# Kernel tuning notes

Measured on AMD Instinct MI355X. Metric: run time of the kernel, lower is better.

## Reference

```python
import jax, jax.numpy as jnp
import numpy as np

N_ATOMS = 200_000
N_EDGES = 6_400_000
N_IMAGES = 128


def setup_inputs() -> dict:
    key = jax.random.key(0)
    k1, k2, k3, k4, k5 = jax.random.split(key, 5)
    edge_diff = jax.random.normal(k1, (N_EDGES, 3), dtype=jnp.float32)
    dE_ddiff = jax.random.normal(k2, (N_EDGES, 3), dtype=jnp.float32)
    # cells: perturbed identity cells so volumes are well-conditioned
    cell = jnp.eye(3, dtype=jnp.float32) * 10.0 + 0.1 * jax.random.normal(
        k3, (N_IMAGES, 3, 3), dtype=jnp.float32)
    edge_idx = jax.random.randint(k4, (N_EDGES, 2), 0, N_ATOMS, dtype=jnp.int64)
    image_idx = jnp.sort(jax.random.randint(k5, (N_ATOMS,), 0, N_IMAGES, dtype=jnp.int64))
    return {"edge_diff": edge_diff, "dE_ddiff": dE_ddiff, "cell": cell,
            "edge_idx": edge_idx, "image_idx": image_idx}


def reference(edge_diff, dE_ddiff, cell, edge_idx, image_idx):
    idx_i = edge_idx[:, 0]
    idx_j = edge_idx[:, 1]
    # forces: scatter-add +dE to i atoms and -dE to j atoms
    i_forces = jax.ops.segment_sum(dE_ddiff, idx_i, num_segments=N_ATOMS)
    j_forces = jax.ops.segment_sum(-dE_ddiff, idx_j, num_segments=N_ATOMS)
    forces = i_forces + j_forces  # [N_ATOMS, 3]
    # per-edge virial outer product, scattered to atoms then to images
    edge_virial = edge_diff[:, :, None] * dE_ddiff[:, None, :]  # [E,3,3]
    atomic_virial = jax.ops.segment_sum(edge_virial, idx_i, num_segments=N_ATOMS)
    virial = jax.ops.segment_sum(atomic_virial, image_idx, num_segments=N_IMAGES)  # [B,3,3]
    # cell volumes: a . (b x c)
    volumes = jnp.sum(cell[:, 0] * jnp.cross(cell[:, 1], cell[:, 2]), axis=-1)  # [B]
    stress = -virial / volumes[:, None, None]
    return forces, virial, stress
```

## Files before the change

### kernel.cpp

```cpp
#include <hip/hip_runtime.h>
#include <hip/hip_fp16.h>


typedef unsigned int uint;
typedef unsigned short ushort;

#define SLICES  256
#define BASHIFT 8
#define NBCAP   1024
#define NVMAX   1152

__device__ __forceinline__ uint2 pack_entry(float dx, float dy, float dz, uint local) {
    const __half2 hxy = __floats2half2_rn(dx, dy);
    const ushort  hz  = __half_as_ushort(__float2half_rn(dz));
    uint2 r;
    r.x = *(const uint*)&hxy;
    r.y = (uint)hz | (local << 16);
    return r;
}

__global__ __launch_bounds__(1024) void k_count(
    const int2* __restrict__ edge_idx, uint* __restrict__ counts,
    int n_edges, int es, int nb)
{
    __shared__ uint hist[NBCAP];
    for (int t = threadIdx.x; t < nb; t += blockDim.x) hist[t] = 0;
    __syncthreads();
    const int s  = blockIdx.x;
    const int e0 = s * es;
    const int e1 = min(n_edges, e0 + es);
    for (int e = e0 + threadIdx.x; e < e1; e += blockDim.x) {
        const int2 ij = edge_idx[e];
        atomicAdd(&hist[((uint)ij.x) >> BASHIFT], 1u);
        atomicAdd(&hist[((uint)ij.y) >> BASHIFT], 1u);
    }
    __syncthreads();
    for (int b = threadIdx.x; b < nb; b += blockDim.x)
        counts[(size_t)b * SLICES + s] = hist[b];
}

__global__ __launch_bounds__(SLICES) void k_rowsum(
    const uint* __restrict__ counts, uint* __restrict__ rowsum)
{
    __shared__ uint red[SLICES];
    const int b = blockIdx.x;
    red[threadIdx.x] = counts[(size_t)b * SLICES + threadIdx.x];
    __syncthreads();
    for (int off = SLICES / 2; off > 0; off >>= 1) {
        if (threadIdx.x < off) red[threadIdx.x] += red[threadIdx.x + off];
        __syncthreads();
    }
    if (threadIdx.x == 0) rowsum[b] = red[0];
}

__global__ __launch_bounds__(1024) void k_scan_rows(
    const uint* __restrict__ rowsum, uint* __restrict__ rowoff, int nb)
{
    __shared__ uint psum[1024];
    const int t = threadIdx.x;
    psum[t] = (t < nb) ? rowsum[t] : 0u;
    __syncthreads();
    for (int off = 1; off < 1024; off <<= 1) {
        uint v = (t >= off) ? psum[t - off] : 0u;
        __syncthreads();
        psum[t] += v;
        __syncthreads();
    }
    if (t < nb) rowoff[t] = (t == 0) ? 0u : psum[t - 1];
}

__global__ __launch_bounds__(SLICES) void k_rowscan(
    uint* __restrict__ counts, const uint* __restrict__ rowoff)
{
    __shared__ uint psum[SLICES];
    const int b = blockIdx.x;
    const int t = threadIdx.x;
    const uint c = counts[(size_t)b * SLICES + t];
    psum[t] = c;
    __syncthreads();
    for (int off = 1; off < SLICES; off <<= 1) {
        uint v = (t >= off) ? psum[t - off] : 0u;
        __syncthreads();
        psum[t] += v;
        __syncthreads();
    }
    counts[(size_t)b * SLICES + t] = rowoff[b] + psum[t] - c;
}

__global__ __launch_bounds__(1024) void k_scatter(
    const float* __restrict__ edge_diff, const float* __restrict__ dE_ddiff,
    const int2* __restrict__ edge_idx, const int* __restrict__ image_idx,
    const uint* __restrict__ offsets, uint2* __restrict__ entries,
    float* __restrict__ virial , int n_edges, int es, int nb, int nv)
{
    __shared__ uint  cur[NBCAP];
    __shared__ float lv[NVMAX];
    const int s = blockIdx.x;
    for (int t = threadIdx.x; t < nb; t += blockDim.x)
        cur[t] = offsets[(size_t)t * SLICES + s];
    for (int t = threadIdx.x; t < nv; t += blockDim.x) lv[t] = 0.f;
    __syncthreads();

    const int e0 = s * es;
    const int e1 = min(n_edges, e0 + es);
    for (int e = e0 + threadIdx.x; e < e1; e += blockDim.x) {
        const int2 ij = edge_idx[e];
        const float dx = dE_ddiff[3*e + 0];
        const float dy = dE_ddiff[3*e + 1];
        const float dz = dE_ddiff[3*e + 2];

        const uint ai = (uint)ij.x, aj = (uint)ij.y;
        const uint pi = atomicAdd(&cur[ai >> BASHIFT], 1u);
        entries[pi] = pack_entry(dx, dy, dz, ai & ((1u << BASHIFT) - 1u));
        const uint pj = atomicAdd(&cur[aj >> BASHIFT], 1u);
        entries[pj] = pack_entry(-dx, -dy, -dz, aj & ((1u << BASHIFT) - 1u));

        const float ex = edge_diff[3*e + 0];
        const float ey = edge_diff[3*e + 1];
        const float ez = edge_diff[3*e + 2];
        float* v = &lv[image_idx[ai] * 9];
        atomicAdd(&v[0], ex*dx); atomicAdd(&v[1], ex*dy); atomicAdd(&v[2], ex*dz);
        atomicAdd(&v[3], ey*dx); atomicAdd(&v[4], ey*dy); atomicAdd(&v[5], ey*dz);
        atomicAdd(&v[6], ez*dx); atomicAdd(&v[7], ez*dy); atomicAdd(&v[8], ez*dz);
    }
    __syncthreads();
    for (int t = threadIdx.x; t < nv; t += blockDim.x) {
        const float val = lv[t];
        if (val != 0.f) unsafeAtomicAdd(&virial[t], val);
    }
}

__global__ __launch_bounds__(256) void k_gather(
    const uint2* __restrict__ entries, const uint* __restrict__ offsets,
    float* __restrict__ forces, int n_atoms, int nb, uint total)
{
    __shared__ float tile[3 << BASHIFT];
    const int q = blockIdx.x;
    for (int t = threadIdx.x; t < (3 << BASHIFT); t += blockDim.x) tile[t] = 0.f;
    __syncthreads();

    const uint beg = offsets[(size_t)q * SLICES];
    const uint end = (q + 1 < nb) ? offsets[(size_t)(q + 1) * SLICES] : total;
    for (uint k = beg + threadIdx.x; k < end; k += blockDim.x) {
        const uint2 ent = entries[k];
        const float2 xy = __half22float2(*(const __half2*)&ent.x);
        const float  z  = __half2float(__ushort_as_half((ushort)(ent.y & 0xffffu)));
        const uint local = ent.y >> 16;
        atomicAdd(&tile[local*3 + 0], xy.x);
        atomicAdd(&tile[local*3 + 1], xy.y);
        atomicAdd(&tile[local*3 + 2], z);
    }
    __syncthreads();

    const int base = q << BASHIFT;
    const int lim3 = min(n_atoms - base, 1 << BASHIFT) * 3;
    for (int t = threadIdx.x; t < lim3; t += blockDim.x)
        forces[(size_t)base * 3 + t] = tile[t];
}

__global__ void k_stress(const float* __restrict__ cell,
                         const float* __restrict__ virial,
                         float* __restrict__ stress, int n_images)
{
    const int t = blockIdx.x * blockDim.x + threadIdx.x;
    if (t >= n_images * 9) return;
    const float* c = &cell[(t / 9) * 9];
    const float crx = c[4]*c[8] - c[5]*c[7];
    const float cry = c[5]*c[6] - c[3]*c[8];
    const float crz = c[3]*c[7] - c[4]*c[6];
    const float vol = c[0]*crx + c[1]*cry + c[2]*crz;
    stress[t] = virial[t] * (-1.0f / vol);
}

__global__ __launch_bounds__(256) void edge_kernel_fb(
    const float* __restrict__ edge_diff, const float* __restrict__ dE_ddiff,
    const int2* __restrict__ edge_idx, const int* __restrict__ image_idx,
    float* __restrict__ forces, float* __restrict__ virial,
    int n_edges, int n_images)
{
    extern __shared__ float lds_v[];
    const int nv = n_images * 9;
    for (int t = threadIdx.x; t < nv; t += blockDim.x) lds_v[t] = 0.f;
    __syncthreads();
    const int stride = gridDim.x * blockDim.x;
    for (int e = blockIdx.x * blockDim.x + threadIdx.x; e < n_edges; e += stride) {
        const int2 ij = edge_idx[e];
        const int i = ij.x, j = ij.y;
        const float dx = dE_ddiff[3*e+0], dy = dE_ddiff[3*e+1], dz = dE_ddiff[3*e+2];
        unsafeAtomicAdd(&forces[3*i+0],  dx);
        unsafeAtomicAdd(&forces[3*i+1],  dy);
        unsafeAtomicAdd(&forces[3*i+2],  dz);
        unsafeAtomicAdd(&forces[3*j+0], -dx);
        unsafeAtomicAdd(&forces[3*j+1], -dy);
        unsafeAtomicAdd(&forces[3*j+2], -dz);
        const float ex = edge_diff[3*e+0], ey = edge_diff[3*e+1], ez = edge_diff[3*e+2];
        float* v = &lds_v[image_idx[i] * 9];
        atomicAdd(&v[0], ex*dx); atomicAdd(&v[1], ex*dy); atomicAdd(&v[2], ex*dz);
        atomicAdd(&v[3], ey*dx); atomicAdd(&v[4], ey*dy); atomicAdd(&v[5], ey*dz);
        atomicAdd(&v[6], ez*dx); atomicAdd(&v[7], ez*dy); atomicAdd(&v[8], ez*dz);
    }
    __syncthreads();
    for (int t = threadIdx.x; t < nv; t += blockDim.x) {
        const float val = lds_v[t];
        if (val != 0.f) unsafeAtomicAdd(&virial[t], val);
    }
}

extern "C" void kernel_launch(void* const* d_in, const int* in_sizes, int n_in,
                              void* d_out, int out_size, void* d_ws, size_t ws_size,
                              hipStream_t stream)
{
    const float* edge_diff = (const float*)d_in[0];
    const float* dE_ddiff  = (const float*)d_in[1];
    const float* cell      = (const float*)d_in[2];
    const int2*  edge_idx  = (const int2*)d_in[3];
    const int*   image_idx = (const int*)d_in[4];

    const int n_edges  = in_sizes[0] / 3;
    const int n_images = in_sizes[2] / 9;
    const int n_atoms  = in_sizes[4];
    const int nv       = n_images * 9;

    float* out    = (float*)d_out;
    float* forces = out;
    float* virial = out + (size_t)n_atoms * 3;
    float* stress = virial + nv;

    const int nb = (n_atoms + (1 << BASHIFT) - 1) >> BASHIFT;
    const int es = (n_edges + SLICES - 1) / SLICES;
    const uint total = (uint)(2 * (size_t)n_edges);

    const size_t entries_bytes = (size_t)total * sizeof(uint2);
    const size_t counts_bytes  = (size_t)nb * SLICES * sizeof(uint);
    const size_t aux_bytes     = 2 * (size_t)NBCAP * sizeof(uint);
    const size_t need = entries_bytes + counts_bytes + aux_bytes;

    if (ws_size >= need && nb <= NBCAP && nv <= NVMAX) {
        uint2* entries = (uint2*)d_ws;
        uint*  offsets = (uint*)((char*)d_ws + entries_bytes);
        uint*  rowsum  = offsets + (size_t)nb * SLICES;
        uint*  rowoff  = rowsum + NBCAP;

        hipMemsetAsync(virial, 0, nv * sizeof(float), stream);

        k_count<<<SLICES, 1024, 0, stream>>>(edge_idx, offsets, n_edges, es, nb);
        k_rowsum<<<nb, SLICES, 0, stream>>>(offsets, rowsum);
        k_scan_rows<<<1, 1024, 0, stream>>>(rowsum, rowoff, nb);
        k_rowscan<<<nb, SLICES, 0, stream>>>(offsets, rowoff);
        k_scatter<<<SLICES, 1024, 0, stream>>>(edge_diff, dE_ddiff, edge_idx, image_idx,
                                               offsets, entries, virial, n_edges, es, nb, nv);
        k_gather<<<nb, 256, 0, stream>>>(entries, offsets, forces, n_atoms, nb, total);
        k_stress<<<(nv + 255) / 256, 256, 0, stream>>>(cell, virial, stress, n_images);
    } else {
        hipMemsetAsync(out, 0, ((size_t)n_atoms * 3 + nv) * sizeof(float), stream);
        edge_kernel_fb<<<2048, 256, nv * sizeof(float), stream>>>(
            edge_diff, dE_ddiff, edge_idx, image_idx, forces, virial, n_edges, n_images);
        k_stress<<<(nv + 255) / 256, 256, 0, stream>>>(cell, virial, stress, n_images);
    }
}
```

Baseline: 731.8 us.

## Stage scatter entries in shared memory by bucket before global writes; per-wave gather tiles

The scatter kernel now processes edges in chunks of 4096. It counts entries per bucket in shared memory, prefix-sums the counts, and sorts the packed entries locally so the global writes to each bucket come out contiguous instead of random. The aim is fewer scattered global stores, paid for with more shared memory, a 1024-step scan and extra barriers per chunk. The gather kernel also gives each wave its own shared accumulation tile, summed at the end, to reduce LDS atomic contention.

```diff
diff --git a/kernel.cpp b/kernel.cpp
--- a/kernel.cpp
+++ b/kernel.cpp
@@ -9,6 +9,8 @@
 #define BASHIFT 8
 #define NBCAP   1024
 #define NVMAX   1152
+#define CHUNK_E 4096
+#define CHUNK_ENT (2*CHUNK_E)
 
 __device__ __forceinline__ uint2 pack_entry(float dx, float dy, float dz, uint local) {
     const __half2 hxy = __floats2half2_rn(dx, dy);
@@ -93,38 +95,94 @@
     const uint* __restrict__ offsets, uint2* __restrict__ entries,
     float* __restrict__ virial , int n_edges, int es, int nb, int nv)
 {
-    __shared__ uint  cur[NBCAP];
+    __shared__ uint2 s_ent[CHUNK_ENT];
+    __shared__ uint  s_dst[CHUNK_ENT];
+    __shared__ uint  cnt[NBCAP];
+    __shared__ uint  base[NBCAP];
+    __shared__ uint  tmp[1024];
+    __shared__ uint  gcur[NBCAP];
     __shared__ float lv[NVMAX];
-    const int s = blockIdx.x;
-    for (int t = threadIdx.x; t < nb; t += blockDim.x)
-        cur[t] = offsets[(size_t)t * SLICES + s];
-    for (int t = threadIdx.x; t < nv; t += blockDim.x) lv[t] = 0.f;
+
+    const int s   = blockIdx.x;
+    const int tid = threadIdx.x;
+
+    for (int t = tid; t < nb; t += 1024) gcur[t] = offsets[(size_t)t * SLICES + s];
+    for (int t = tid; t < nv; t += 1024) lv[t] = 0.f;
     __syncthreads();
 
     const int e0 = s * es;
     const int e1 = min(n_edges, e0 + es);
-    for (int e = e0 + threadIdx.x; e < e1; e += blockDim.x) {
-        const int2 ij = edge_idx[e];
-        const float dx = dE_ddiff[3*e + 0];
-        const float dy = dE_ddiff[3*e + 1];
-        const float dz = dE_ddiff[3*e + 2];
-
-        const uint ai = (uint)ij.x, aj = (uint)ij.y;
-        const uint pi = atomicAdd(&cur[ai >> BASHIFT], 1u);
-        entries[pi] = pack_entry(dx, dy, dz, ai & ((1u << BASHIFT) - 1u));
-        const uint pj = atomicAdd(&cur[aj >> BASHIFT], 1u);
-        entries[pj] = pack_entry(-dx, -dy, -dz, aj & ((1u << BASHIFT) - 1u));
-
-        const float ex = edge_diff[3*e + 0];
-        const float ey = edge_diff[3*e + 1];
-        const float ez = edge_diff[3*e + 2];
-        float* v = &lv[image_idx[ai] * 9];
-        atomicAdd(&v[0], ex*dx); atomicAdd(&v[1], ex*dy); atomicAdd(&v[2], ex*dz);
-        atomicAdd(&v[3], ey*dx); atomicAdd(&v[4], ey*dy); atomicAdd(&v[5], ey*dz);
-        atomicAdd(&v[6], ez*dx); atomicAdd(&v[7], ez*dy); atomicAdd(&v[8], ez*dz);
-    }
-    __syncthreads();
-    for (int t = threadIdx.x; t < nv; t += blockDim.x) {
+
+    for (int clo = e0; clo < e1; clo += CHUNK_E) {
+        const int chi  = min(e1, clo + CHUNK_E);
+        const int nent = 2 * (chi - clo);
+
+        cnt[tid] = 0;
+        __syncthreads();
+
+        uint2 ent_i[4], ent_j[4];
+        uint  bi[4], bj[4], ri[4], rj[4];
+        #pragma unroll
+        for (int k = 0; k < 4; ++k) {
+            const int e = clo + (k << 10) + tid;
+            bi[k] = 0xffffffffu;
+            if (e < chi) {
+                const int2 ij = edge_idx[e];
+                const float dx = dE_ddiff[3*e + 0];
+                const float dy = dE_ddiff[3*e + 1];
+                const float dz = dE_ddiff[3*e + 2];
+                const uint ai = (uint)ij.x, aj = (uint)ij.y;
+                bi[k] = ai >> BASHIFT;
+                bj[k] = aj >> BASHIFT;
+                ent_i[k] = pack_entry( dx,  dy,  dz, ai & ((1u << BASHIFT) - 1u));
+                ent_j[k] = pack_entry(-dx, -dy, -dz, aj & ((1u << BASHIFT) - 1u));
+                ri[k] = atomicAdd(&cnt[bi[k]], 1u);
+                rj[k] = atomicAdd(&cnt[bj[k]], 1u);
+
+                const float ex = edge_diff[3*e + 0];
+                const float ey = edge_diff[3*e + 1];
+                const float ez = edge_diff[3*e + 2];
+                float* v = &lv[image_idx[ai] * 9];
+                atomicAdd(&v[0], ex*dx); atomicAdd(&v[1], ex*dy); atomicAdd(&v[2], ex*dz);
+                atomicAdd(&v[3], ey*dx); atomicAdd(&v[4], ey*dy); atomicAdd(&v[5], ey*dz);
+                atomicAdd(&v[6], ez*dx); atomicAdd(&v[7], ez*dy); atomicAdd(&v[8], ez*dz);
+            }
+        }
+        __syncthreads();
+
+        const uint c0 = cnt[tid];
+        tmp[tid] = c0;
+        __syncthreads();
+        for (int off = 1; off < 1024; off <<= 1) {
+            const uint v = (tid >= off) ? tmp[tid - off] : 0u;
+            __syncthreads();
+            tmp[tid] += v;
+            __syncthreads();
+        }
+        base[tid] = tmp[tid] - c0;
+        __syncthreads();
+
+        #pragma unroll
+        for (int k = 0; k < 4; ++k) {
+            if (bi[k] != 0xffffffffu) {
+                const uint pi = base[bi[k]] + ri[k];
+                s_ent[pi] = ent_i[k];
+                s_dst[pi] = gcur[bi[k]] + ri[k];
+                const uint pj = base[bj[k]] + rj[k];
+                s_ent[pj] = ent_j[k];
+                s_dst[pj] = gcur[bj[k]] + rj[k];
+            }
+        }
+        __syncthreads();
+
+        for (int t = tid; t < nent; t += 1024)
+            entries[s_dst[t]] = s_ent[t];
+
+        gcur[tid] += cnt[tid];
+        __syncthreads();
+    }
+
+    for (int t = tid; t < nv; t += 1024) {
         const float val = lv[t];
         if (val != 0.f) unsafeAtomicAdd(&virial[t], val);
     }
@@ -134,28 +192,31 @@
     const uint2* __restrict__ entries, const uint* __restrict__ offsets,
     float* __restrict__ forces, int n_atoms, int nb, uint total)
 {
-    __shared__ float tile[3 << BASHIFT];
-    const int q = blockIdx.x;
-    for (int t = threadIdx.x; t < (3 << BASHIFT); t += blockDim.x) tile[t] = 0.f;
+    __shared__ float tile[4][3 << BASHIFT];
+    const int q   = blockIdx.x;
+    const int wid = threadIdx.x >> 6;
+    for (int t = threadIdx.x; t < 4 * (3 << BASHIFT); t += blockDim.x)
+        ((float*)tile)[t] = 0.f;
     __syncthreads();
 
     const uint beg = offsets[(size_t)q * SLICES];
     const uint end = (q + 1 < nb) ? offsets[(size_t)(q + 1) * SLICES] : total;
+    float* wt = tile[wid];
     for (uint k = beg + threadIdx.x; k < end; k += blockDim.x) {
         const uint2 ent = entries[k];
         const float2 xy = __half22float2(*(const __half2*)&ent.x);
         const float  z  = __half2float(__ushort_as_half((ushort)(ent.y & 0xffffu)));
         const uint local = ent.y >> 16;
-        atomicAdd(&tile[local*3 + 0], xy.x);
-        atomicAdd(&tile[local*3 + 1], xy.y);
-        atomicAdd(&tile[local*3 + 2], z);
+        atomicAdd(&wt[local*3 + 0], xy.x);
+        atomicAdd(&wt[local*3 + 1], xy.y);
+        atomicAdd(&wt[local*3 + 2], z);
     }
     __syncthreads();
 
     const int base = q << BASHIFT;
     const int lim3 = min(n_atoms - base, 1 << BASHIFT) * 3;
     for (int t = threadIdx.x; t < lim3; t += blockDim.x)
-        forces[(size_t)base * 3 + t] = tile[t];
+        forces[(size_t)base * 3 + t] = tile[0][t] + tile[1][t] + tile[2][t] + tile[3][t];
 }
 
 __global__ void k_stress(const float* __restrict__ cell,
```

Result: slower. 768.7 us (+5.0%).
